# Optimization experiments

Hardware: AMD Instinct MI355X
Metric: run time of the kernel (lower is better)

## Reference

```python
import jax, jax.numpy as jnp
import numpy as np

B, S, D, H = 8, 1024, 512, 8  # batch, max_mol_real, d_model, num_heads
DH = D // 2                   # per-branch width
DEPTH = D // H                # per-head depth (64)
HH = H // 2                   # heads per branch (4)


def setup_inputs() -> dict:
    key = jax.random.key(0)
    ks = jax.random.split(key, 16)
    sc = 0.02
    inp = {
        'x': jax.random.normal(ks[0], (B, S, D), jnp.float32),
        'mask': jnp.zeros((B, 1, 1, S), jnp.float32),
        'adj': jax.random.uniform(ks[1], (B, S, S), jnp.float32),
        'dist': jax.random.uniform(ks[2], (B, S, S), jnp.float32),
        # dist branch projections (Dense(d_model/2))
        'Wq_dist': jax.random.normal(ks[3], (D, DH), jnp.float32) * sc,
        'bq_dist': jnp.zeros((DH,), jnp.float32),
        'Wk_dist': jax.random.normal(ks[4], (D, DH), jnp.float32) * sc,
        'bk_dist': jnp.zeros((DH,), jnp.float32),
        'Wv_dist': jax.random.normal(ks[5], (D, DH), jnp.float32) * sc,
        'bv_dist': jnp.zeros((DH,), jnp.float32),
        # adj branch projections
        'Wq_adj': jax.random.normal(ks[6], (D, DH), jnp.float32) * sc,
        'bq_adj': jnp.zeros((DH,), jnp.float32),
        'Wk_adj': jax.random.normal(ks[7], (D, DH), jnp.float32) * sc,
        'bk_adj': jnp.zeros((DH,), jnp.float32),
        'Wv_adj': jax.random.normal(ks[8], (D, DH), jnp.float32) * sc,
        'bv_adj': jnp.zeros((DH,), jnp.float32),
        # output projection Dense(d_model)
        'Wo': jax.random.normal(ks[9], (D, D), jnp.float32) * sc,
        'bo': jnp.zeros((D,), jnp.float32),
    }
    return inp


def _split_heads(t):
    # (B, S, HH*DEPTH) -> (B, HH, S, DEPTH)
    return t.reshape(B, S, HH, DEPTH).transpose(0, 2, 1, 3)


def _sdpa_ad(q, k, v, mask, adj=None, dist=None):
    # mask: (B,1,1,S) -> additive -1e9 * mask, per original code
    m = mask * -1000000000.0
    logits = jnp.einsum('bhqd,bhkd->bhqk', q, k) / jnp.sqrt(jnp.float32(DEPTH))
    w = jax.nn.softmax(logits + m, axis=-1)  # (B, HH, S, S)
    if adj is not None:
        w = w * adj[:, None, :, :]
    if dist is not None:  # dist_value == 'original'
        w = w * jax.nn.softmax(dist[:, None, :, :] + m, axis=-1)
    return jnp.einsum('bhqk,bhkd->bhqd', w, v)


def reference(x, mask, adj, dist,
              Wq_dist, bq_dist, Wk_dist, bk_dist, Wv_dist, bv_dist,
              Wq_adj, bq_adj, Wk_adj, bk_adj, Wv_adj, bv_adj,
              Wo, bo):
    # ----- dist branch -----
    qd = _split_heads(x @ Wq_dist + bq_dist)
    kd = _split_heads(x @ Wk_dist + bk_dist)
    vd = _split_heads(x @ Wv_dist + bv_dist)
    od = _sdpa_ad(qd, kd, vd, mask, adj=None, dist=dist)
    od = od.transpose(0, 2, 1, 3).reshape(B, S, DH)
    # ----- adj branch -----
    qa = _split_heads(x @ Wq_adj + bq_adj)
    ka = _split_heads(x @ Wk_adj + bk_adj)
    va = _split_heads(x @ Wv_adj + bv_adj)
    oa = _sdpa_ad(qa, ka, va, mask, adj=adj, dist=None)
    oa = oa.transpose(0, 2, 1, 3).reshape(B, S, DH)
    # ----- concat + output dense -----
    cat = jnp.concatenate([od, oa], axis=-1)  # (B, S, D)
    return cat @ Wo + bo
```

## Files before the change

### kernel.cpp

```cpp
#include <hip/hip_runtime.h>

typedef __attribute__((ext_vector_type(8))) short bf16x8;
typedef __attribute__((ext_vector_type(4))) float f32x4;
typedef unsigned short ushortT;

#define B_   8
#define S_   1024
#define D_   512
#define DH_  256
#define NH_  4
#define DEP_ 64
#define LOG2E 1.4426950408889634f

__device__ __forceinline__ unsigned short f2bf(float f){
    unsigned u = __builtin_bit_cast(unsigned, f);
    u += 0x7fffu + ((u>>16)&1u);
    return (unsigned short)(u>>16);
}
__device__ __forceinline__ float bf2f(ushortT v){
    unsigned u = ((unsigned)v)<<16;
    return __builtin_bit_cast(float, u);
}
__device__ __forceinline__ unsigned fbits(float f){ return __builtin_bit_cast(unsigned, f); }
__device__ __forceinline__ int swz(int row,int cb){ return (row<<7) + (cb ^ ((row&7)<<4)); }

__global__ __launch_bounds__(256) void prep_x(const float* __restrict__ x, ushortT* __restrict__ xb){
    size_t t = (size_t)blockIdx.x*256 + threadIdx.x;
    float4 v = *(const float4*)(x + t*4);
    ushort4 o; o.x=f2bf(v.x); o.y=f2bf(v.y); o.z=f2bf(v.z); o.w=f2bf(v.w);
    *(ushort4*)(xb + t*4) = o;
}

__global__ __launch_bounds__(256) void prep_w(
    const float* __restrict__ W0, const float* __restrict__ W1, const float* __restrict__ W2,
    const float* __restrict__ W3, const float* __restrict__ W4, const float* __restrict__ W5,
    const float* __restrict__ B0, const float* __restrict__ B1, const float* __restrict__ B2,
    const float* __restrict__ B3, const float* __restrict__ B4, const float* __restrict__ B5,
    ushortT* __restrict__ Wt, float* __restrict__ bias_all)
{
    int t = blockIdx.x*256 + threadIdx.x;
    int k = t / 384;
    int n4 = (t - k*384)*4;
#pragma unroll
    for (int j=0;j<4;++j){
        int n = n4+j; int mat = n>>8, nc = n&255;
        const float* Wp = (mat==0)?W0:(mat==1)?W1:(mat==2)?W2:(mat==3)?W3:(mat==4)?W4:W5;
        Wt[(size_t)n*512 + k] = f2bf(Wp[(size_t)k*256 + nc]);
    }
    if (t < 384){
#pragma unroll
        for (int j=0;j<4;++j){
            int n = n4+j; int mat = n>>8, nc = n&255;
            const float* Bp = (mat==0)?B0:(mat==1)?B1:(mat==2)?B2:(mat==3)?B3:(mat==4)?B4:B5;
            bias_all[n] = Bp[nc];
        }
    }
}

__global__ __launch_bounds__(256) void prep_wo(const float* __restrict__ Wo, ushortT* __restrict__ Wot){
    __shared__ float t[32][33];
    const int k0 = blockIdx.y*32, n0 = blockIdx.x*32;
    const int ty = threadIdx.x>>5, tx = threadIdx.x&31;
#pragma unroll
    for (int i=0;i<4;++i)
        t[ty+8*i][tx] = Wo[(size_t)(k0+ty+8*i)*512 + n0+tx];
    __syncthreads();
#pragma unroll
    for (int i=0;i<4;++i)
        Wot[(size_t)(n0+ty+8*i)*512 + k0+tx] = f2bf(t[tx][ty+8*i]);
}

__global__ __launch_bounds__(256) void dist_sm(
    const float* __restrict__ dist, const float* __restrict__ mask, ushortT* __restrict__ Md)
{
    __shared__ ushortT pl[16][1032];
    const int bx = blockIdx.x;
    const int w = bx&3, qb = (bx>>2)&15, b = bx>>6;
    const int wd = threadIdx.x>>6, lane = threadIdx.x&63;
    const float* mrow = mask + (size_t)b*S_;

    for (int rr=0; rr<4; ++rr){
        const int er = 4*wd + rr;
        const int q = qb*64 + 16*w + er;
        const float* drow = dist + ((size_t)(b*1024 + q))*S_;
        float v[16];
        float mx = -1e30f;
#pragma unroll
        for (int j=0;j<4;++j){
            const int idx = j*256 + lane*4;
            float4 d = *(const float4*)(drow + idx);
            float4 mk = *(const float4*)(mrow + idx);
            v[j*4+0] = fmaf(mk.x, -1e9f, d.x); v[j*4+1] = fmaf(mk.y, -1e9f, d.y);
            v[j*4+2] = fmaf(mk.z, -1e9f, d.z); v[j*4+3] = fmaf(mk.w, -1e9f, d.w);
#pragma unroll
            for (int i=0;i<4;++i) mx = fmaxf(mx, v[j*4+i]);
        }
        mx = fmaxf(mx, __shfl_xor(mx,1));  mx = fmaxf(mx, __shfl_xor(mx,2));
        mx = fmaxf(mx, __shfl_xor(mx,4));  mx = fmaxf(mx, __shfl_xor(mx,8));
        mx = fmaxf(mx, __shfl_xor(mx,16)); mx = fmaxf(mx, __shfl_xor(mx,32));
        float s = 0.f;
#pragma unroll
        for (int i=0;i<16;++i){ v[i] = __builtin_exp2f((v[i]-mx)*LOG2E); s += v[i]; }
        s += __shfl_xor(s,1);  s += __shfl_xor(s,2);  s += __shfl_xor(s,4);
        s += __shfl_xor(s,8);  s += __shfl_xor(s,16); s += __shfl_xor(s,32);
        const float rcp = 1.f/s;
#pragma unroll
        for (int j=0;j<4;++j){
            ushort4 o;
            o.x=f2bf(v[j*4+0]*rcp); o.y=f2bf(v[j*4+1]*rcp);
            o.z=f2bf(v[j*4+2]*rcp); o.w=f2bf(v[j*4+3]*rcp);
            *(ushort4*)(&pl[er][j*256 + lane*4]) = o;
        }
    }
    __syncthreads();

    const int t = threadIdx.x;
    const int e2 = (t>>2)&15, kt2 = t&3, g2 = t>>6;
    ushortT* slab = Md + (((size_t)(b*16+qb)*16)*4 + w)*1024;
#pragma unroll
    for (int s2=0;s2<16;++s2){
        ushort4 vv = *(const ushort4*)(&pl[e2][64*s2 + 16*kt2 + 4*g2]);
        *(ushort4*)(slab + (size_t)s2*4096 + t*4) = vv;
    }
}

__global__ __launch_bounds__(256) void shuf_adj(
    const float* __restrict__ adj, ushortT* __restrict__ Ma)
{
    __shared__ ushortT tl[64][72];
    const int bx = blockIdx.x;
    const int s = bx&15, qb = (bx>>4)&15, b = bx>>8;
    const int t = threadIdx.x;
    {
        const int qr = t>>2, c0 = (t&3)*16;
        const float* src = adj + ((size_t)(b*1024 + qb*64 + qr))*S_ + 64*s + c0;
#pragma unroll
        for (int i=0;i<4;++i){
            float4 d = *(const float4*)(src + 4*i);
            tl[qr][c0+4*i+0]=f2bf(d.x); tl[qr][c0+4*i+1]=f2bf(d.y);
            tl[qr][c0+4*i+2]=f2bf(d.z); tl[qr][c0+4*i+3]=f2bf(d.w);
        }
    }
    __syncthreads();
    const int w2 = t>>6, l = t&63, g = l>>4, e = l&15;
    ushortT o[16];
#pragma unroll
    for (int kt=0;kt<4;++kt)
        *(ushort4*)(&o[4*kt]) = *(const ushort4*)(&tl[16*w2 + e][16*kt + 4*g]);
    ushortT* dst = Ma + ((((size_t)(b*16+qb)*16 + s)*4 + w2)*1024) + l*16;
    *(uint4*)(dst)     = *(uint4*)(&o[0]);
    *(uint4*)(dst + 8) = *(uint4*)(&o[8]);
}

__global__ __launch_bounds__(256) void qkv_mfma(
    const ushortT* __restrict__ xb, const ushortT* __restrict__ Wt,
    const float* __restrict__ bias_all,
    ushortT* __restrict__ q_d, ushortT* __restrict__ k_d, ushortT* __restrict__ vt_d,
    ushortT* __restrict__ q_a, ushortT* __restrict__ k_a, ushortT* __restrict__ vt_a)
{
    __shared__ __align__(16) char sm[32768];
    const int tid = threadIdx.x;
    const int w = tid>>6, l = tid&63, g = l>>4, e = l&15;
    const int wm = w>>1, wn = w&1;
    const int n0 = blockIdx.x*128, m0 = blockIdx.y*128;

    f32x4 acc[4][4];
#pragma unroll
    for (int i=0;i<4;++i)
#pragma unroll
        for (int j=0;j<4;++j) acc[i][j] = (f32x4){0.f,0.f,0.f,0.f};

    for (int k0=0;k0<512;k0+=64){
        __syncthreads();
#pragma unroll
        for (int i=0;i<4;++i){
            int fi = tid + i*256;
            int row = fi>>3, f = fi&7;
            *(uint4*)(sm + swz(row, f*16))         = *(const uint4*)(xb + ((size_t)(m0+row)*512 + k0 + 8*f));
            *(uint4*)(sm + 16384 + swz(row, f*16)) = *(const uint4*)(Wt + ((size_t)(n0+row)*512 + k0 + 8*f));
        }
        __syncthreads();
#pragma unroll
        for (int c=0;c<2;++c){
            bf16x8 a[4];
#pragma unroll
            for (int mt=0;mt<4;++mt)
                a[mt] = *(const bf16x8*)(sm + swz(64*wm + 16*mt + e, g*16 + 64*c));
#pragma unroll
            for (int nt=0;nt<4;++nt){
                bf16x8 bfr = *(const bf16x8*)(sm + 16384 + swz(64*wn + 16*nt + e, g*16 + 64*c));
#pragma unroll
                for (int mt=0;mt<4;++mt)
                    acc[mt][nt] = __builtin_amdgcn_mfma_f32_16x16x32_bf16(a[mt], bfr, acc[mt][nt], 0,0,0);
            }
        }
    }

    const int mat = n0>>8;
    const int nb  = n0 + 64*wn;
    const int h   = (nb&255)>>6;
    const int mb  = m0 + 64*wm;
    const int b   = mb>>10, s0 = mb&1023;
    ushortT* base = (mat==0)?q_d:(mat==1)?k_d:(mat==2)?vt_d:(mat==3)?q_a:(mat==4)?k_a:vt_a;
    const bool isV = (mat==2)||(mat==5);

    float bi[4];
#pragma unroll
    for (int nt=0;nt<4;++nt) bi[nt] = bias_all[nb + 16*nt + e];

    __syncthreads();
    char* qd = sm + w*8192;
#pragma unroll
    for (int nt=0;nt<4;++nt){
#pragma unroll
        for (int mt=0;mt<4;++mt){
#pragma unroll
            for (int r=0;r<4;++r){
                const int row = 16*mt + 4*g + r;
                const int col = 16*nt + e;
                const int lr = isV ? col : row;
                const int lc = isV ? row : col;
                *(ushortT*)(qd + swz(lr, lc*2)) = f2bf(acc[mt][nt][r] + bi[nt]);
            }
        }
    }
    const int rrb = l>>3, dq = l&7;
#pragma unroll
    for (int pass=0;pass<8;++pass){
        const int rr = pass*8 + rrb;
        uint4 vv = *(const uint4*)(qd + swz(rr, dq*16));
        const size_t off = isV ? ((size_t)((b*NH_+h)*DEP_ + rr)*S_ + s0 + dq*8)
                               : ((size_t)((b*NH_+h)*S_ + s0 + rr)*DEP_ + dq*8);
        *(uint4*)(base + off) = vv;
    }
}

__global__ __launch_bounds__(256,4) void attn_mfma(
    const ushortT* __restrict__ q_d, const ushortT* __restrict__ k_d, const ushortT* __restrict__ vt_d,
    const ushortT* __restrict__ q_a, const ushortT* __restrict__ k_a, const ushortT* __restrict__ vt_a,
    const ushortT* __restrict__ Md, const ushortT* __restrict__ Ma,
    const float* __restrict__ mask, ushortT* __restrict__ cat)
{
    __shared__ __align__(16) char sm[28672];
    float* Msk = (float*)(sm + 24576);

    const int tid = threadIdx.x;
    const int w = tid>>6, l = tid&63, g = l>>4, e = l&15;
    const int bz = blockIdx.y;
    const int br = bz>>5;
    const int bh = bz&31, b = bh>>2, h = bh&3;
    const int qb = blockIdx.x;
    const int q0 = qb*64;

    const ushortT* Qg = br ? q_a  : q_d;
    const ushortT* Kg = br ? k_a  : k_d;
    const ushortT* Vg = br ? vt_a : vt_d;

    const ushortT* Qb = Qg + ((size_t)bh*S_ + q0)*DEP_;
    const ushortT* Kb = Kg + (size_t)bh*S_*DEP_;
    const ushortT* Vb = Vg + (size_t)bh*DEP_*S_;
    const ushortT* Mbase = (br ? Ma : Md) + ((size_t)((b*16+qb)*16)*4 + w)*1024 + l*16;
    const float*   mkb = mask + (size_t)b*S_;

    const int srow = tid>>3, sf = tid&7;
    const int srow2 = srow+32;

    bf16x8 aq0 = *(const bf16x8*)(Qb + (size_t)(16*w+e)*DEP_ + 8*g);
    bf16x8 aq1 = *(const bf16x8*)(Qb + (size_t)(16*w+e)*DEP_ + 8*g + 32);

    for (int i=tid;i<S_;i+=256) Msk[i] = mkb[i] * (-1e9f*LOG2E);

    uint4 kreg0 = *(const uint4*)(Kb + (size_t)srow*DEP_ + 8*sf);
    uint4 kreg1 = *(const uint4*)(Kb + (size_t)srow2*DEP_ + 8*sf);
    uint4 vreg0 = *(const uint4*)(Vb + (size_t)srow*S_  + 8*sf);
    uint4 vreg1 = *(const uint4*)(Vb + (size_t)srow2*S_ + 8*sf);
    bf16x8 mc0 = *(const bf16x8*)(Mbase);
    bf16x8 mc1 = *(const bf16x8*)(Mbase + 8);

    float zl = 0.f;
    f32x4 oacc[4];
#pragma unroll
    for (int dt=0;dt<4;++dt) oacc[dt] = (f32x4){0.f,0.f,0.f,0.f};

    for (int s=0;s<16;++s){
        const int k0 = s*64;
        __syncthreads();
        *(uint4*)(sm +        swz(srow,  sf*16)) = kreg0;
        *(uint4*)(sm +        swz(srow2, sf*16)) = kreg1;
        *(uint4*)(sm + 8192 + swz(srow,  sf*16)) = vreg0;
        *(uint4*)(sm + 8192 + swz(srow2, sf*16)) = vreg1;
        __syncthreads();

        const int kn = (s<15) ? k0+64 : 0;
        kreg0 = *(const uint4*)(Kb + (size_t)(kn+srow)*DEP_ + 8*sf);
        kreg1 = *(const uint4*)(Kb + (size_t)(kn+srow2)*DEP_ + 8*sf);
        vreg0 = *(const uint4*)(Vb + (size_t)srow*S_  + kn + 8*sf);
        vreg1 = *(const uint4*)(Vb + (size_t)srow2*S_ + kn + 8*sf);
        const size_t mo = (size_t)((s<15)?s+1:0)*4096;
        bf16x8 mn0 = *(const bf16x8*)(Mbase + mo);
        bf16x8 mn1 = *(const bf16x8*)(Mbase + mo + 8);

        f32x4 lg[4];
#pragma unroll
        for (int kt=0;kt<4;++kt) lg[kt] = (f32x4){0.f,0.f,0.f,0.f};
        __builtin_amdgcn_s_setprio(1);
#pragma unroll
        for (int kt=0;kt<4;++kt){
            bf16x8 bk0 = *(const bf16x8*)(sm + swz(16*kt + e, g*16));
            bf16x8 bk1 = *(const bf16x8*)(sm + swz(16*kt + e, g*16 + 64));
            lg[kt] = __builtin_amdgcn_mfma_f32_16x16x32_bf16(bk0, aq0, lg[kt], 0,0,0);
            lg[kt] = __builtin_amdgcn_mfma_f32_16x16x32_bf16(bk1, aq1, lg[kt], 0,0,0);
        }
        __builtin_amdgcn_s_setprio(0);

        f32x4 mskv[4];
#pragma unroll
        for (int kt=0;kt<4;++kt)
            mskv[kt] = *(const f32x4*)(Msk + k0 + 16*kt + 4*g);

#pragma unroll
        for (int kt=0;kt<4;++kt){
            float e1[4], pm[4];
#pragma unroll
            for (int r=0;r<4;++r)
                e1[r] = __builtin_exp2f(fmaf(lg[kt][r], 0.125f*LOG2E, mskv[kt][r]));
            zl += (e1[0]+e1[1]) + (e1[2]+e1[3]);
#pragma unroll
            for (int r=0;r<4;++r){
                const int j = 4*kt + r;
                const float mj = bf2f((ushortT)(j<8 ? mc0[j] : mc1[j-8]));
                pm[r] = e1[r]*mj;
            }
            unsigned w0 = __builtin_amdgcn_perm(fbits(pm[1]), fbits(pm[0]), 0x07060302u);
            unsigned w1 = __builtin_amdgcn_perm(fbits(pm[3]), fbits(pm[2]), 0x07060302u);
            *(unsigned*)(sm + 16384 + 2048*w + swz(e, 32*kt + 8*g))     = w0;
            *(unsigned*)(sm + 16384 + 2048*w + swz(e, 32*kt + 8*g + 4)) = w1;
        }
        mc0 = mn0; mc1 = mn1;

        __builtin_amdgcn_s_setprio(1);
#pragma unroll
        for (int c=0;c<2;++c){
            bf16x8 ap = *(const bf16x8*)(sm + 16384 + 2048*w + swz(e, g*16 + 64*c));
#pragma unroll
            for (int dt=0;dt<4;++dt){
                bf16x8 bv = *(const bf16x8*)(sm + 8192 + swz(16*dt + e, g*16 + 64*c));
                oacc[dt] = __builtin_amdgcn_mfma_f32_16x16x32_bf16(ap, bv, oacc[dt], 0,0,0);
            }
        }
        __builtin_amdgcn_s_setprio(0);
    }

    zl += __shfl_xor(zl,16); zl += __shfl_xor(zl,32);
    float inv[4];
#pragma unroll
    for (int r=0;r<4;++r)
        inv[r] = 1.f / __shfl(zl, (l & 48) | (4*g + r));

    const int coff = br*DH_;
#pragma unroll
    for (int dt=0;dt<4;++dt){
#pragma unroll
        for (int r=0;r<4;++r){
            int q = q0 + 16*w + 4*g + r;
            int c = coff + h*DEP_ + 16*dt + e;
            cat[((size_t)b*S_ + q)*D_ + c] = f2bf(oacc[dt][r]*inv[r]);
        }
    }
}

__global__ __launch_bounds__(256) void out_mfma(
    const ushortT* __restrict__ catb, const ushortT* __restrict__ Wot,
    const float* __restrict__ bo, float* __restrict__ out)
{
    __shared__ __align__(16) char sm[32768];
    const int tid = threadIdx.x;
    const int w = tid>>6, l = tid&63, g = l>>4, e = l&15;
    const int wm = w>>1, wn = w&1;
    const int n0 = blockIdx.x*128, m0 = blockIdx.y*128;

    f32x4 acc[4][4];
#pragma unroll
    for (int i=0;i<4;++i)
#pragma unroll
        for (int j=0;j<4;++j) acc[i][j] = (f32x4){0.f,0.f,0.f,0.f};

    for (int k0=0;k0<512;k0+=64){
        __syncthreads();
#pragma unroll
        for (int i=0;i<4;++i){
            int fi = tid + i*256;
            int row = fi>>3, f = fi&7;
            *(uint4*)(sm + swz(row, f*16))         = *(const uint4*)(catb + ((size_t)(m0+row)*512 + k0 + 8*f));
            *(uint4*)(sm + 16384 + swz(row, f*16)) = *(const uint4*)(Wot  + ((size_t)(n0+row)*512 + k0 + 8*f));
        }
        __syncthreads();
#pragma unroll
        for (int c=0;c<2;++c){
            bf16x8 a[4];
#pragma unroll
            for (int mt=0;mt<4;++mt)
                a[mt] = *(const bf16x8*)(sm + swz(64*wm + 16*mt + e, g*16 + 64*c));
#pragma unroll
            for (int nt=0;nt<4;++nt){
                bf16x8 bfr = *(const bf16x8*)(sm + 16384 + swz(64*wn + 16*nt + e, g*16 + 64*c));
#pragma unroll
                for (int mt=0;mt<4;++mt)
                    acc[mt][nt] = __builtin_amdgcn_mfma_f32_16x16x32_bf16(a[mt], bfr, acc[mt][nt], 0,0,0);
            }
        }
    }

#pragma unroll
    for (int nt=0;nt<4;++nt){
        int n = n0 + 64*wn + 16*nt + e;
        float bi = bo[n];
#pragma unroll
        for (int mt=0;mt<4;++mt){
#pragma unroll
            for (int r=0;r<4;++r){
                int m = m0 + 64*wm + 16*mt + 4*g + r;
                out[(size_t)m*512 + n] = acc[mt][nt][r] + bi;
            }
        }
    }
}

extern "C" void kernel_launch(void* const* d_in, const int* in_sizes, int n_in,
                              void* d_out, int out_size, void* d_ws, size_t ws_size,
                              hipStream_t stream)
{
    (void)in_sizes; (void)n_in; (void)out_size; (void)ws_size;

    const float* x    = (const float*)d_in[0];
    const float* mask = (const float*)d_in[1];
    const float* adj  = (const float*)d_in[2];
    const float* dist = (const float*)d_in[3];
    const float* Wqd  = (const float*)d_in[4];  const float* bqd = (const float*)d_in[5];
    const float* Wkd  = (const float*)d_in[6];  const float* bkd = (const float*)d_in[7];
    const float* Wvd  = (const float*)d_in[8];  const float* bvd = (const float*)d_in[9];
    const float* Wqa  = (const float*)d_in[10]; const float* bqa = (const float*)d_in[11];
    const float* Wka  = (const float*)d_in[12]; const float* bka = (const float*)d_in[13];
    const float* Wva  = (const float*)d_in[14]; const float* bva = (const float*)d_in[15];
    const float* Wo   = (const float*)d_in[16]; const float* bo  = (const float*)d_in[17];
    float* out = (float*)d_out;

    char* W = (char*)d_ws;
    ushortT* xb   = (ushortT*)(W + 0);
    ushortT* catb = (ushortT*)(W + 0);
    ushortT* Wt   = (ushortT*)(W + 8388608);
    ushortT* Ma   = (ushortT*)(W + 8388608);
    ushortT* Wot  = (ushortT*)(W + 8388608);
    float*   bias = (float*)  (W + 9961472);
    ushortT* q_d  = (ushortT*)(W + 25165824);
    ushortT* k_d  = (ushortT*)(W + 29360128);
    ushortT* vt_d = (ushortT*)(W + 33554432);
    ushortT* q_a  = (ushortT*)(W + 37748736);
    ushortT* k_a  = (ushortT*)(W + 41943040);
    ushortT* vt_a = (ushortT*)(W + 46137344);
    ushortT* Md   = (ushortT*)(W + 50331648);

    prep_x<<<4096, 256, 0, stream>>>(x, xb);
    prep_w<<<768, 256, 0, stream>>>(Wqd,Wkd,Wvd,Wqa,Wka,Wva,
                                    bqd,bkd,bvd,bqa,bka,bva, Wt, bias);
    dist_sm<<<512, 256, 0, stream>>>(dist, mask, Md);
    qkv_mfma<<<dim3(12,64), 256, 0, stream>>>(xb, Wt, bias, q_d,k_d,vt_d, q_a,k_a,vt_a);
    shuf_adj<<<2048, 256, 0, stream>>>(adj, Ma);
    attn_mfma<<<dim3(16,64), 256, 0, stream>>>(q_d,k_d,vt_d, q_a,k_a,vt_a,
                                               Md, Ma, mask, catb);
    prep_wo<<<dim3(16,16), 256, 0, stream>>>(Wo, Wot);
    out_mfma<<<dim3(4,64), 256, 0, stream>>>(catb, Wot, bo, out);
}
```

Measured before the change: 119.4 us.

## Permute key ordering so softmax probabilities feed PV MFMA directly from registers

The K tile rows are stored into shared memory in a permuted (sigma) order, and the mask/adjacency slabs and mask reads use matching permuted column offsets. With that ordering, each lane's four QK^T output fragments line up with the A-operand layout of the PV MFMA, so the packed bf16 probabilities are assembled in registers instead of being written to and re-read from a per-wave LDS buffer. This removes the P round-trip through LDS and shrinks shared memory, which could allow more resident blocks. The cost is correctness depending on the permutation being consistent across the prep kernels, the K staging and the V ordering.

```diff
diff --git a/kernel.cpp b/kernel.cpp
--- a/kernel.cpp
+++ b/kernel.cpp
@@ -2,6 +2,7 @@
 
 typedef __attribute__((ext_vector_type(8))) short bf16x8;
 typedef __attribute__((ext_vector_type(4))) float f32x4;
+typedef __attribute__((ext_vector_type(4))) unsigned u32x4;
 typedef unsigned short ushortT;
 
 #define B_   8
@@ -23,6 +24,9 @@
 }
 __device__ __forceinline__ unsigned fbits(float f){ return __builtin_bit_cast(unsigned, f); }
 __device__ __forceinline__ int swz(int row,int cb){ return (row<<7) + (cb ^ ((row&7)<<4)); }
+__device__ __forceinline__ int sigrow(int sr){
+    return 16*((sr>>5) + 2*((sr>>2)&1)) + 4*((sr>>3)&3) + (sr&3);
+}
 
 __global__ __launch_bounds__(256) void prep_x(const float* __restrict__ x, ushortT* __restrict__ xb){
     size_t t = (size_t)blockIdx.x*256 + threadIdx.x;
@@ -116,10 +120,11 @@
 
     const int t = threadIdx.x;
     const int e2 = (t>>2)&15, kt2 = t&3, g2 = t>>6;
+    const int koff = 32*(kt2&1) + 4*(kt2>>1) + 8*g2;
     ushortT* slab = Md + (((size_t)(b*16+qb)*16)*4 + w)*1024;
 #pragma unroll
     for (int s2=0;s2<16;++s2){
-        ushort4 vv = *(const ushort4*)(&pl[e2][64*s2 + 16*kt2 + 4*g2]);
+        ushort4 vv = *(const ushort4*)(&pl[e2][64*s2 + koff]);
         *(ushort4*)(slab + (size_t)s2*4096 + t*4) = vv;
     }
 }
@@ -146,7 +151,7 @@
     ushortT o[16];
 #pragma unroll
     for (int kt=0;kt<4;++kt)
-        *(ushort4*)(&o[4*kt]) = *(const ushort4*)(&tl[16*w2 + e][16*kt + 4*g]);
+        *(ushort4*)(&o[4*kt]) = *(const ushort4*)(&tl[16*w2 + e][32*(kt&1) + 4*(kt>>1) + 8*g]);
     ushortT* dst = Ma + ((((size_t)(b*16+qb)*16 + s)*4 + w2)*1024) + l*16;
     *(uint4*)(dst)     = *(uint4*)(&o[0]);
     *(uint4*)(dst + 8) = *(uint4*)(&o[8]);
@@ -241,8 +246,8 @@
     const ushortT* __restrict__ Md, const ushortT* __restrict__ Ma,
     const float* __restrict__ mask, ushortT* __restrict__ cat)
 {
-    __shared__ __align__(16) char sm[28672];
-    float* Msk = (float*)(sm + 24576);
+    __shared__ __align__(16) char sm[20480];
+    float* Msk = (float*)(sm + 16384);
 
     const int tid = threadIdx.x;
     const int w = tid>>6, l = tid&63, g = l>>4, e = l&15;
@@ -264,6 +269,8 @@
 
     const int srow = tid>>3, sf = tid&7;
     const int srow2 = srow+32;
+    const int krow  = sigrow(srow);
+    const int krow2 = sigrow(srow2);
 
     bf16x8 aq0 = *(const bf16x8*)(Qb + (size_t)(16*w+e)*DEP_ + 8*g);
     bf16x8 aq1 = *(const bf16x8*)(Qb + (size_t)(16*w+e)*DEP_ + 8*g + 32);
@@ -285,8 +292,8 @@
     for (int s=0;s<16;++s){
         const int k0 = s*64;
         __syncthreads();
-        *(uint4*)(sm +        swz(srow,  sf*16)) = kreg0;
-        *(uint4*)(sm +        swz(srow2, sf*16)) = kreg1;
+        *(uint4*)(sm +        swz(krow,  sf*16)) = kreg0;
+        *(uint4*)(sm +        swz(krow2, sf*16)) = kreg1;
         *(uint4*)(sm + 8192 + swz(srow,  sf*16)) = vreg0;
         *(uint4*)(sm + 8192 + swz(srow2, sf*16)) = vreg1;
         __syncthreads();
@@ -313,17 +320,14 @@
         }
         __builtin_amdgcn_s_setprio(0);
 
-        f32x4 mskv[4];
-#pragma unroll
-        for (int kt=0;kt<4;++kt)
-            mskv[kt] = *(const f32x4*)(Msk + k0 + 16*kt + 4*g);
-
+        unsigned pw[8];
 #pragma unroll
         for (int kt=0;kt<4;++kt){
+            const f32x4 mskv = *(const f32x4*)(Msk + k0 + 32*(kt&1) + 4*(kt>>1) + 8*g);
             float e1[4], pm[4];
 #pragma unroll
             for (int r=0;r<4;++r)
-                e1[r] = __builtin_exp2f(fmaf(lg[kt][r], 0.125f*LOG2E, mskv[kt][r]));
+                e1[r] = __builtin_exp2f(fmaf(lg[kt][r], 0.125f*LOG2E, mskv[r]));
             zl += (e1[0]+e1[1]) + (e1[2]+e1[3]);
 #pragma unroll
             for (int r=0;r<4;++r){
@@ -331,22 +335,24 @@
                 const float mj = bf2f((ushortT)(j<8 ? mc0[j] : mc1[j-8]));
                 pm[r] = e1[r]*mj;
             }
-            unsigned w0 = __builtin_amdgcn_perm(fbits(pm[1]), fbits(pm[0]), 0x07060302u);
-            unsigned w1 = __builtin_amdgcn_perm(fbits(pm[3]), fbits(pm[2]), 0x07060302u);
-            *(unsigned*)(sm + 16384 + 2048*w + swz(e, 32*kt + 8*g))     = w0;
-            *(unsigned*)(sm + 16384 + 2048*w + swz(e, 32*kt + 8*g + 4)) = w1;
+            pw[2*kt]   = __builtin_amdgcn_perm(fbits(pm[1]), fbits(pm[0]), 0x07060302u);
+            pw[2*kt+1] = __builtin_amdgcn_perm(fbits(pm[3]), fbits(pm[2]), 0x07060302u);
         }
         mc0 = mn0; mc1 = mn1;
 
+        const bf16x8 ap0 = __builtin_bit_cast(bf16x8, (u32x4){pw[0],pw[1],pw[4],pw[5]});
+        const bf16x8 ap1 = __builtin_bit_cast(bf16x8, (u32x4){pw[2],pw[3],pw[6],pw[7]});
+
         __builtin_amdgcn_s_setprio(1);
 #pragma unroll
-        for (int c=0;c<2;++c){
-            bf16x8 ap = *(const bf16x8*)(sm + 16384 + 2048*w + swz(e, g*16 + 64*c));
-#pragma unroll
-            for (int dt=0;dt<4;++dt){
-                bf16x8 bv = *(const bf16x8*)(sm + 8192 + swz(16*dt + e, g*16 + 64*c));
-                oacc[dt] = __builtin_amdgcn_mfma_f32_16x16x32_bf16(ap, bv, oacc[dt], 0,0,0);
-            }
+        for (int dt=0;dt<4;++dt){
+            bf16x8 bv0 = *(const bf16x8*)(sm + 8192 + swz(16*dt + e, g*16));
+            oacc[dt] = __builtin_amdgcn_mfma_f32_16x16x32_bf16(ap0, bv0, oacc[dt], 0,0,0);
+        }
+#pragma unroll
+        for (int dt=0;dt<4;++dt){
+            bf16x8 bv1 = *(const bf16x8*)(sm + 8192 + swz(16*dt + e, g*16 + 64));
+            oacc[dt] = __builtin_amdgcn_mfma_f32_16x16x32_bf16(ap1, bv1, oacc[dt], 0,0,0);
         }
         __builtin_amdgcn_s_setprio(0);
     }
```

Result: no change. 117.4 us (-1.6%).
